# Performance work log

Hardware: AMD Instinct MI355X
Metric: run time of the kernel (lower is better)

The kernel has to match this reference:

```python
import jax, jax.numpy as jnp
import numpy as np

B = 128; DIM_IN = 3; MAX_CYCLE = 50; NODES = 18
T = MAX_CYCLE * NODES          # cycle_size = 900
F1, F2 = 32, 64                # stgcn_filters
NCLS = 3
N = B * T                      # nodes seen by GATv2 = 115200
E = 12 * N                     # edges (avg degree 12)
EPS = 1e-5


def setup_inputs() -> dict:
    key = jax.random.key(0)
    keys = iter(jax.random.split(key, 48))
    def p(shape, scale=0.05):
        return jax.random.normal(next(keys), shape, jnp.float32) * scale
    inp = {}
    inp["x"] = jax.random.normal(next(keys), (B, DIM_IN, T), jnp.float32)
    inp["edge_index"] = jax.random.randint(next(keys), (2, E), 0, N)
    def block(pfx, cin, c):
        inp[pfx + "_tc1_w"] = p((c, cin, 5)); inp[pfx + "_tc1_b"] = p((c,))
        inp[pfx + "_wl"] = p((c, c)); inp[pfx + "_bl"] = p((c,))
        inp[pfx + "_wr"] = p((c, c)); inp[pfx + "_br"] = p((c,))
        inp[pfx + "_att"] = p((c,)); inp[pfx + "_gbias"] = p((c,))
        inp[pfx + "_bn_g"] = jnp.ones((c,), jnp.float32)
        inp[pfx + "_bn_b"] = jnp.zeros((c,), jnp.float32)
        inp[pfx + "_tc2_w"] = p((c, c, 5)); inp[pfx + "_tc2_b"] = p((c,))
    block("b1", DIM_IN, F1)
    block("b2", F1, F2)
    inp["fc1_w"] = p((128, T * F2), 0.01); inp["fc1_b"] = p((128,))
    inp["hbn1_g"] = jnp.ones((128,), jnp.float32); inp["hbn1_b"] = jnp.zeros((128,), jnp.float32)
    inp["fc2_w"] = p((64, 128)); inp["fc2_b"] = p((64,))
    inp["hbn2_g"] = jnp.ones((64,), jnp.float32); inp["hbn2_b"] = jnp.zeros((64,), jnp.float32)
    inp["fc3_w"] = p((NCLS, 64)); inp["fc3_b"] = p((NCLS,))
    return inp


def _conv1d_same(x, w, b):
    # x: [B, Cin, T], w: [Cout, Cin, 5], 'same' padding (pad 2/2)
    y = jax.lax.conv_general_dilated(x, w, (1,), [(2, 2)],
                                     dimension_numbers=("NCH", "OIH", "NCH"))
    return y + b[None, :, None]


def _bn(h, g, b):
    # BatchNorm1d on [N, C] with batch statistics
    m = h.mean(0)
    v = h.var(0)
    return (h - m) * jax.lax.rsqrt(v + EPS) * g + b


def _gatv2(h, src, dst, wl, bl, wr, br, att, gbias):
    # PyG GATv2Conv, heads=1, negative_slope=0.2, self loops already in src/dst
    xl = h @ wl.T + bl            # source transform, also the message
    xr = h @ wr.T + br            # target transform
    e = jnp.dot(jax.nn.leaky_relu(xl[src] + xr[dst], 0.2), att)  # [E]
    m = jax.ops.segment_max(e, dst, num_segments=N)
    ex = jnp.exp(e - m[dst])
    s = jax.ops.segment_sum(ex, dst, num_segments=N)
    alpha = ex / s[dst]
    out = jax.ops.segment_sum(alpha[:, None] * xl[src], dst, num_segments=N)
    return out + gbias


def _block(x, src, dst, tc1_w, tc1_b, wl, bl, wr, br, att, gbias, bn_g, bn_b, tc2_w, tc2_b):
    x = jax.nn.relu(_conv1d_same(x, tc1_w, tc1_b))      # [B, C, T]
    C = tc1_w.shape[0]
    h = x.reshape(T * B, C)                             # torch .view(T*B, C) (raw row-major)
    h = jax.nn.relu(_gatv2(h, src, dst, wl, bl, wr, br, att, gbias))
    h = _bn(h, bn_g, bn_b)
    h = h.reshape(B, C, T)                              # torch .view(B, C, T)
    return jax.nn.relu(_conv1d_same(h, tc2_w, tc2_b))


def reference(x, edge_index,
              b1_tc1_w, b1_tc1_b, b1_wl, b1_bl, b1_wr, b1_br, b1_att, b1_gbias,
              b1_bn_g, b1_bn_b, b1_tc2_w, b1_tc2_b,
              b2_tc1_w, b2_tc1_b, b2_wl, b2_bl, b2_wr, b2_br, b2_att, b2_gbias,
              b2_bn_g, b2_bn_b, b2_tc2_w, b2_tc2_b,
              fc1_w, fc1_b, hbn1_g, hbn1_b, fc2_w, fc2_b, hbn2_g, hbn2_b, fc3_w, fc3_b):
    sl = jnp.arange(N, dtype=edge_index.dtype)          # PyG add_self_loops=True
    src = jnp.concatenate([edge_index[0], sl])
    dst = jnp.concatenate([edge_index[1], sl])
    h = _block(x, src, dst, b1_tc1_w, b1_tc1_b, b1_wl, b1_bl, b1_wr, b1_br,
               b1_att, b1_gbias, b1_bn_g, b1_bn_b, b1_tc2_w, b1_tc2_b)
    h = jax.nn.relu(h)                                  # extra relu on non-final block (dropout off)
    h = _block(h, src, dst, b2_tc1_w, b2_tc1_b, b2_wl, b2_bl, b2_wr, b2_br,
               b2_att, b2_gbias, b2_bn_g, b2_bn_b, b2_tc2_w, b2_tc2_b)
    h = h.reshape(B, F2 * T)
    h = jax.nn.relu(h @ fc1_w.T + fc1_b)
    h = _bn(h, hbn1_g, hbn1_b)
    h = jax.nn.relu(h @ fc2_w.T + fc2_b)
    h = _bn(h, hbn2_g, hbn2_b)
    logits = h @ fc3_w.T + fc3_b
    return (jax.nn.sigmoid(logits), logits)
```

## Files before the change

### kernel.cpp

```cpp
#include <hip/hip_runtime.h>
#include <hip/hip_bf16.h>

typedef __hip_bfloat16 bf16;
typedef __attribute__((ext_vector_type(8))) short s16x8;
typedef __attribute__((ext_vector_type(4))) float f32x4;
#define DEV static __device__ __forceinline__

DEV float b2f(bf16 v){ return __bfloat162float(v); }
DEV bf16  f2b(float v){ return __float2bfloat16(v); }
DEV int   is_f32(const void* gones){ return ((const unsigned int*)gones)[0] == 0x3F800000u ? 1 : 0; }
DEV float ldin(const void* p, int f32, int i){
    return f32 ? ((const float*)p)[i] : __bfloat162float(((const bf16*)p)[i]);
}
DEV void unpk(unsigned u, float& a, float& b){
    a = __uint_as_float(u << 16);
    b = __uint_as_float(u & 0xffff0000u);
}
DEV float lrelu(float t){ return fmaxf(t, 0.f) + 0.2f * fminf(t, 0.f); }
DEV unsigned short bfu(float v){ bf16 h = f2b(v); return *(unsigned short*)&h; }
DEV float ldT(const float* p, int i){ return p[i]; }
DEV float ldT(const bf16*  p, int i){ return b2f(p[i]); }
DEV void st4(float* d, float4 o){ *(float4*)d = o; }
DEV void st1(float* d, float v){ *d = v; }
DEV void st4(bf16* d, float4 o){
    unsigned short ob[4] = {bfu(o.x), bfu(o.y), bfu(o.z), bfu(o.w)};
    *(ushort4*)d = *(ushort4*)ob;
}
DEV void st1(bf16* d, float v){ *d = f2b(v); }

constexpr int Bb  = 128;
constexpr int Tt  = 900;
constexpr int Nn  = Bb * Tt;
constexpr int Ee  = 12 * Nn;
constexpr int CAP = 48;
constexpr int NBK  = 256;
constexpr int NPB  = Nn / NBK;
constexpr int BCAP = 8192;
constexpr int WROWS = 96 + 1024 + 2048 + 4096;
constexpr int WTOT  = WROWS * 5;
constexpr int WBF   = 5120 + 10240 + 20480;
constexpr int WXT   = 2*32*32 + 64 + 2*64*64 + 128;

__global__ __launch_bounds__(256) void k_wprep(const void* wa, const void* wb_, const void* wc,
    const void* wd,
    const void* b1wl, const void* b1bl, const void* b1wr, const void* b1br,
    const void* b2wl, const void* b2bl, const void* b2wr, const void* b2br,
    const void* gones, float* __restrict__ wp, bf16* __restrict__ wbf,
    float* __restrict__ wx, int* __restrict__ gcur){
    const int f32 = is_f32(gones);
    if (blockIdx.x == 0 && threadIdx.x < NBK) gcur[threadIdx.x] = 0;
    int e = blockIdx.x * 256 + threadIdx.x;
    if (e < WTOT){
        int r = e / 5, k = e - r * 5;
        const void* src; int rb;
        if (r < 96)      { src = wa; rb = 0; }
        else if (r < 1120){ src = wb_; rb = 96; }
        else if (r < 3168){ src = wc; rb = 1120; }
        else             { src = wd; rb = 3168; }
        wp[r * 8 + k] = ldin(src, f32, (r - rb) * 5 + k);
    } else if (e < WTOT + WBF){
        int e2 = e - WTOT;
        const void* src; int kk, r;
        if (e2 < 5120)      { kk = e2 >> 10; r = e2 & 1023; src = wb_; }
        else if (e2 < 15360){ int e3 = e2 - 5120;  kk = e3 >> 11; r = e3 & 2047; src = wc; }
        else                { int e3 = e2 - 15360; kk = e3 >> 12; r = e3 & 4095; src = wd; }
        wbf[e2] = f2b(ldin(src, f32, r * 5 + kk));
    } else if (e < WTOT + WBF + WXT){
        int e3 = e - WTOT - WBF;
        float v;
        if      (e3 < 1024){ int t = e3;         int c = t >> 5, f = t & 31; v = ldin(b1wl, f32, f * 32 + c); }
        else if (e3 < 2048){ int t = e3 - 1024;  int c = t >> 5, f = t & 31; v = ldin(b1wr, f32, f * 32 + c); }
        else if (e3 < 2080)  v = ldin(b1bl, f32, e3 - 2048);
        else if (e3 < 2112)  v = ldin(b1br, f32, e3 - 2080);
        else if (e3 < 6208){ int t = e3 - 2112;  int c = t >> 6, f = t & 63; v = ldin(b2wl, f32, f * 64 + c); }
        else if (e3 < 10304){int t = e3 - 6208;  int c = t >> 6, f = t & 63; v = ldin(b2wr, f32, f * 64 + c); }
        else if (e3 < 10368) v = ldin(b2bl, f32, e3 - 10304);
        else                 v = ldin(b2br, f32, e3 - 10368);
        wx[e3] = v;
    }
}

__global__ __launch_bounds__(256) void k_bucket(const int* __restrict__ ei,
                                                int* __restrict__ gcur, int2* __restrict__ bkt){
    constexpr int TILE = 4096;
    const int base = blockIdx.x * TILE;
    const int tid = threadIdx.x;
    __shared__ int cnt[NBK];
    __shared__ int gbase[NBK];
    cnt[tid] = 0;
    __syncthreads();
    int es[16], er[16], eb[16], rk[16];
    #pragma unroll
    for (int k = 0; k < 16; ++k){
        int idx = base + k * 256 + tid;
        if (idx < Ee){
            es[k] = ei[idx];
            int d = ei[Ee + idx];
            eb[k] = d / NPB;
            er[k] = d - eb[k] * NPB;
            rk[k] = atomicAdd(&cnt[eb[k]], 1);
        } else eb[k] = -1;
    }
    __syncthreads();
    {
        int c = cnt[tid];
        gbase[tid] = (c > 0) ? atomicAdd(&gcur[tid], c) : 0;
    }
    __syncthreads();
    #pragma unroll
    for (int k = 0; k < 16; ++k){
        if (eb[k] >= 0){
            int slot = gbase[eb[k]] + rk[k];
            if (slot < BCAP)
                bkt[(size_t)eb[k] * BCAP + slot] = make_int2(er[k], es[k]);
        }
    }
}

__global__ __launch_bounds__(256) void k_csr2(const int2* __restrict__ bkt, const int* __restrict__ gcur,
                                              int* __restrict__ csr, int* __restrict__ cnt){
    const int b = blockIdx.x;
    const int n0 = b * NPB;
    __shared__ int lcnt[NPB];
    for (int i = threadIdx.x; i < NPB; i += 256) lcnt[i] = 0;
    __syncthreads();
    const int tot = min(gcur[b], BCAP);
    for (int i = threadIdx.x; i < tot; i += 256){
        int2 e = bkt[(size_t)b * BCAP + i];
        int p = atomicAdd(&lcnt[e.x], 1);
        if (p < CAP) csr[(size_t)(n0 + e.x) * CAP + p] = e.y;
    }
    __syncthreads();
    for (int i = threadIdx.x; i < NPB; i += 256) cnt[n0 + i] = lcnt[i];
}

template<bool EXT, int CIN, int COUT, bool BN>
__global__ __launch_bounds__(256) void k_conv(const void* __restrict__ x,
    const float* __restrict__ wp, int wbase,
    const void* __restrict__ bias, const float* __restrict__ scale, const float* __restrict__ shift,
    const void* __restrict__ gones, float* __restrict__ y)
{
    const int f32 = is_f32(gones);
    __shared__ alignas(16) float xs[CIN][132];
    const int b = blockIdx.x >> 3, t0 = (blockIdx.x & 7) * 128;
    const int tid = threadIdx.x;
    for (int i = tid; i < CIN * 132; i += 256){
        int ci = i / 132, tt = i % 132;
        int gt = t0 + tt - 2;
        float v = 0.f;
        if (gt >= 0 && gt < Tt){
            int idx = (b * CIN + ci) * Tt + gt;
            v = EXT ? ldin(x, f32, idx) : ((const float*)x)[idx];
            if (BN){
                int f = (ci * (Tt % CIN) + gt) % CIN;
                v = v * scale[f] + shift[f];
            }
        }
        xs[ci][tt] = v;
    }
    __syncthreads();
    constexpr int HALF = COUT / 2;
    constexpr int NT   = 256 / HALF;
    constexpr int NW   = 128 / (NT * 4);
    const int cop = tid / NT;
    const int tch = tid % NT;
    const int co = cop, co2 = cop + HALF;
    float acc[NW][2][4];
    #pragma unroll
    for (int iw = 0; iw < NW; ++iw)
        #pragma unroll
        for (int h = 0; h < 2; ++h)
            #pragma unroll
            for (int j = 0; j < 4; ++j) acc[iw][h][j] = 0.f;

    const float* w0p = wp + (size_t)(wbase + co  * CIN) * 8;
    const float* w1p = wp + (size_t)(wbase + co2 * CIN) * 8;
    float4 na = *(const float4*)w0p; float na4 = w0p[4];
    float4 nb = *(const float4*)w1p; float nb4 = w1p[4];
    for (int ci = 0; ci < CIN; ++ci){
        const float w0[5] = {na.x, na.y, na.z, na.w, na4};
        const float w1[5] = {nb.x, nb.y, nb.z, nb.w, nb4};
        if (ci + 1 < CIN){
            const float* p0 = w0p + (size_t)(ci + 1) * 8;
            const float* p1 = w1p + (size_t)(ci + 1) * 8;
            na = *(const float4*)p0; na4 = p0[4];
            nb = *(const float4*)p1; nb4 = p1[4];
        }
        #pragma unroll
        for (int iw = 0; iw < NW; ++iw){
            const int tl = tch * 4 + iw * NT * 4;
            float4 a  = *(const float4*)&xs[ci][tl];
            float4 bq = *(const float4*)&xs[ci][tl + 4];
            float xw[8] = {a.x,a.y,a.z,a.w,bq.x,bq.y,bq.z,bq.w};
            #pragma unroll
            for (int k = 0; k < 5; ++k)
                #pragma unroll
                for (int j = 0; j < 4; ++j){
                    acc[iw][0][j] = fmaf(xw[j + k], w0[k], acc[iw][0][j]);
                    acc[iw][1][j] = fmaf(xw[j + k], w1[k], acc[iw][1][j]);
                }
        }
    }
    const float bv0 = ldin(bias, f32, co), bv1 = ldin(bias, f32, co2);
    #pragma unroll
    for (int iw = 0; iw < NW; ++iw){
        const int t = t0 + tch * 4 + iw * NT * 4;
        if (t < Tt){
            float4 o0, o1;
            o0.x = fmaxf(acc[iw][0][0] + bv0, 0.f); o0.y = fmaxf(acc[iw][0][1] + bv0, 0.f);
            o0.z = fmaxf(acc[iw][0][2] + bv0, 0.f); o0.w = fmaxf(acc[iw][0][3] + bv0, 0.f);
            o1.x = fmaxf(acc[iw][1][0] + bv1, 0.f); o1.y = fmaxf(acc[iw][1][1] + bv1, 0.f);
            o1.z = fmaxf(acc[iw][1][2] + bv1, 0.f); o1.w = fmaxf(acc[iw][1][3] + bv1, 0.f);
            *(float4*)&y[(b * COUT + co ) * Tt + t] = o0;
            *(float4*)&y[(b * COUT + co2) * Tt + t] = o1;
        }
    }
}

template<typename TI, typename TO, int CIN, int COUT, bool BN>
__global__ __launch_bounds__(256) void k_convM(const TI* __restrict__ x, const bf16* __restrict__ wbf,
    int wbase,
    const void* __restrict__ bias, const float* __restrict__ scale, const float* __restrict__ shift,
    const void* __restrict__ gones, TO* __restrict__ y)
{
    const int f32 = is_f32(gones);
    constexpr int STR = CIN + 8;
    constexpr int CI2 = CIN / 2;
    __shared__ alignas(16) float smem[COUT * 132];
    unsigned short* xsT = (unsigned short*)smem;
    const int b = blockIdx.x >> 3, t0 = (blockIdx.x & 7) * 128;
    const int tid = threadIdx.x;
    for (int i = tid; i < CI2 * 128; i += 256){
        int ci2 = i >> 7, tt = i & 127;
        int gt = t0 + tt - 2;
        int ci = ci2 * 2;
        unsigned pack = 0;
        if (gt >= 0 && gt < Tt){
            float v0 = ldT(x, (b * CIN + ci) * Tt + gt);
            float v1 = ldT(x, (b * CIN + ci + 1) * Tt + gt);
            if (BN){
                int fa = (4 * ci + gt) & (CIN - 1), fb = (4 * ci + 4 + gt) & (CIN - 1);
                v0 = v0 * scale[fa] + shift[fa];
                v1 = v1 * scale[fb] + shift[fb];
            }
            pack = (unsigned)bfu(v0) | ((unsigned)bfu(v1) << 16);
        }
        *(unsigned*)&xsT[tt * STR + ci] = pack;
    }
    if (tid < CI2 * 4){
        int ci2 = tid >> 2, tt = 128 + (tid & 3);
        int gt = t0 + tt - 2;
        int ci = ci2 * 2;
        unsigned pack = 0;
        if (gt < Tt){
            float v0 = ldT(x, (b * CIN + ci) * Tt + gt);
            float v1 = ldT(x, (b * CIN + ci + 1) * Tt + gt);
            if (BN){
                int fa = (4 * ci + gt) & (CIN - 1), fb = (4 * ci + 4 + gt) & (CIN - 1);
                v0 = v0 * scale[fa] + shift[fa];
                v1 = v1 * scale[fb] + shift[fb];
            }
            pack = (unsigned)bfu(v0) | ((unsigned)bfu(v1) << 16);
        }
        *(unsigned*)&xsT[tt * STR + ci] = pack;
    }
    __syncthreads();
    const int lane = tid & 63, wid = tid >> 6;
    const int l15 = lane & 15, quad = lane >> 4;
    constexpr int MT  = COUT / 16;
    constexpr int NTP = 2 * MT;
    const int mt  = (MT == 4) ? wid : (wid & 1);
    const int ntb = (MT == 4) ? 0 : (wid >> 1) * NTP;
    const int co0 = mt * 16;
    f32x4 acc[NTP];
    #pragma unroll
    for (int nt = 0; nt < NTP; ++nt){ f32x4 z = {0.f, 0.f, 0.f, 0.f}; acc[nt] = z; }
    for (int kk = 0; kk < 5; ++kk){
        #pragma unroll
        for (int kb = 0; kb < CIN / 32; ++kb){
            s16x8 a = *(const s16x8*)&wbf[wbase + kk * (COUT * CIN) + (co0 + l15) * CIN + kb * 32 + quad * 8];
            #pragma unroll
            for (int nt = 0; nt < NTP; ++nt){
                s16x8 bf = *(const s16x8*)&xsT[((ntb + nt) * 16 + l15 + kk) * STR + kb * 32 + quad * 8];
                acc[nt] = __builtin_amdgcn_mfma_f32_16x16x32_bf16(a, bf, acc[nt], 0, 0, 0);
            }
        }
    }
    __syncthreads();
    #pragma unroll
    for (int nt = 0; nt < NTP; ++nt)
        #pragma unroll
        for (int r = 0; r < 4; ++r)
            smem[(co0 + quad * 4 + r) * 132 + (ntb + nt) * 16 + l15] = acc[nt][r];
    __syncthreads();
    for (int i = tid; i < COUT * 32; i += 256){
        int co = i >> 5, c4 = (i & 31) << 2;
        int t = t0 + c4;
        if (t < Tt){
            float4 o = *(float4*)&smem[co * 132 + c4];
            float bb = ldin(bias, f32, co);
            o.x = fmaxf(o.x + bb, 0.f); o.y = fmaxf(o.y + bb, 0.f);
            o.z = fmaxf(o.z + bb, 0.f); o.w = fmaxf(o.w + bb, 0.f);
            TO* dst = &y[(size_t)(b * COUT + co) * Tt + t];
            if (t + 3 < Tt) st4(dst, o);
            else {
                float ov[4] = {o.x, o.y, o.z, o.w};
                for (int j = 0; j < 4 && t + j < Tt; ++j) st1(dst + j, ov[j]);
            }
        }
    }
}

template<int C>
__global__ __launch_bounds__(256) void k_xlxr(const float* __restrict__ h,
    const float* __restrict__ wx, int wxoff,
    unsigned short* __restrict__ xlh, float* __restrict__ xr,
    double* __restrict__ bnp)
{
    constexpr int NB = 4096 / C;
    constexpr int HS = NB + 4;
    __shared__ alignas(16) float hT[C][HS];
    __shared__ alignas(16) float wlS[C * C];
    __shared__ alignas(16) float wrS[C * C];
    const int tid = threadIdx.x;
    const int n0 = blockIdx.x * NB;
    if (blockIdx.x == 0){
        for (int i = tid; i < 256 * 2 * C; i += 256) bnp[i] = 0.0;
    }
    for (int i = tid; i < NB * C; i += 256){
        int n = i & (NB - 1), c = i / NB;
        hT[c][n] = h[(size_t)(n0 + n) * C + c];
    }
    const float* wl = wx + wxoff;
    const float* wr = wl + C * C;
    for (int i = tid; i < C * C; i += 256){
        wlS[i] = wl[i];
        wrS[i] = wr[i];
    }
    __syncthreads();
    const float* bl = wr + C * C;
    const float* br = bl + C;
    constexpr int FG = C / 4;
    const int fg = tid % FG, ng = tid / FG;
    const int nloc = ng * 4, floc = fg * 4;
    float blv[4], brv[4];
    #pragma unroll
    for (int j = 0; j < 4; ++j){ blv[j] = bl[floc + j]; brv[j] = br[floc + j]; }
    float accL[4][4], accR[4][4];
    #pragma unroll
    for (int i = 0; i < 4; ++i)
        #pragma unroll
        for (int j = 0; j < 4; ++j){ accL[i][j] = 0.f; accR[i][j] = 0.f; }
    #pragma unroll 4
    for (int c = 0; c < C; ++c){
        float4 hv = *(const float4*)&hT[c][nloc];
        float4 lv = *(const float4*)&wlS[c * C + floc];
        float4 rv = *(const float4*)&wrS[c * C + floc];
        float ha[4] = {hv.x,hv.y,hv.z,hv.w};
        float la[4] = {lv.x,lv.y,lv.z,lv.w};
        float ra[4] = {rv.x,rv.y,rv.z,rv.w};
        #pragma unroll
        for (int i = 0; i < 4; ++i)
            #pragma unroll
            for (int j = 0; j < 4; ++j){
                accL[i][j] = fmaf(ha[i], la[j], accL[i][j]);
                accR[i][j] = fmaf(ha[i], ra[j], accR[i][j]);
            }
    }
    #pragma unroll
    for (int i = 0; i < 4; ++i){
        size_t n = n0 + nloc + i;
        bf16 hb[4];
        hb[0] = f2b(accL[i][0] + blv[0]); hb[1] = f2b(accL[i][1] + blv[1]);
        hb[2] = f2b(accL[i][2] + blv[2]); hb[3] = f2b(accL[i][3] + blv[3]);
        *(ushort4*)&xlh[n * C + floc] = *(ushort4*)hb;
        float4 r;
        r.x = accR[i][0] + brv[0]; r.y = accR[i][1] + brv[1];
        r.z = accR[i][2] + brv[2]; r.w = accR[i][3] + brv[3];
        *(float4*)&xr[n * C + floc] = r;
    }
}

template<int L> DEV float rsumL(float v){
    #pragma unroll
    for (int s = L / 2; s > 0; s >>= 1) v += __shfl_xor(v, s, 64);
    return v;
}

template<int C, int FPL>
__global__ __launch_bounds__(256) void k_gat(const unsigned short* __restrict__ xlh,
    const float* __restrict__ xr,
    const int* __restrict__ csr, const int* __restrict__ cnt,
    const void* __restrict__ att, const void* __restrict__ gbias,
    const void* __restrict__ gones, float* __restrict__ out,
    double* __restrict__ bnp)
{
    const int f32 = is_f32(gones);
    constexpr int L   = C / FPL;
    constexpr int NPW = 64 / L;
    const int lane = threadIdx.x & 63, wid = threadIdx.x >> 6;
    const int sub = lane / L, fp = lane % L;
    const int node = (blockIdx.x * 4 + wid) * NPW + sub;
    const int f0 = FPL * fp;
    float xrv[FPL], a1v[FPL], a2v[FPL];
    if constexpr (FPL == 4){
        float4 t = *(const float4*)&xr[(size_t)node * C + f0];
        xrv[0] = t.x; xrv[1] = t.y; xrv[2] = t.z; xrv[3] = t.w;
    } else {
        float2 t = *(const float2*)&xr[(size_t)node * C + f0];
        xrv[0] = t.x; xrv[1] = t.y;
    }
    #pragma unroll
    for (int i = 0; i < FPL; ++i){
        float a = ldin(att, f32, f0 + i);
        a1v[i] = 0.6f * a;
        a2v[i] = 0.4f * a;
    }
    const int deg = min(cnt[node], CAP);
    int degu = deg;
    #pragma unroll
    for (int s = L; s < 64; s <<= 1) degu = max(degu, __shfl_xor(degu, s, 64));

    auto loadv = [&](int s, float (&v)[FPL]){
        if constexpr (FPL == 4){
            uint2 u = *(const uint2*)&xlh[(size_t)s * C + f0];
            unpk(u.x, v[0], v[1]); unpk(u.y, v[2], v[3]);
        } else {
            unsigned u = *(const unsigned*)&xlh[(size_t)s * C + f0];
            unpk(u, v[0], v[1]);
        }
    };
    auto score = [&](const float (&v)[FPL]){
        float l = 0.f;
        #pragma unroll
        for (int i = 0; i < FPL; ++i){
            float t = v[i] + xrv[i];
            l = fmaf(a1v[i], t, l);
            l = fmaf(a2v[i], fabsf(t), l);
        }
        return rsumL<L>(l);
    };

    float ssum, acc[FPL];
    {
        float v[FPL];
        loadv(node, v);
        float w = __expf(score(v));
        ssum = w;
        #pragma unroll
        for (int i = 0; i < FPL; ++i) acc[i] = w * v[i];
    }
    for (int j = 0; j < degu; j += 8){
        const int* crow = &csr[(size_t)node * CAP + j];
        int4 sa = *(const int4*)crow;
        int4 sb = *(const int4*)(crow + 4);
        int ss[8] = {sa.x, sa.y, sa.z, sa.w, sb.x, sb.y, sb.z, sb.w};
        bool av[8];
        #pragma unroll
        for (int q = 0; q < 8; ++q){
            av[q] = (j + q < deg);
            if (!av[q]) ss[q] = node;
        }
        float v[8][FPL];
        #pragma unroll
        for (int q = 0; q < 8; ++q) loadv(ss[q], v[q]);
        float e[8];
        #pragma unroll
        for (int q = 0; q < 8; ++q) e[q] = score(v[q]);
        #pragma unroll
        for (int q = 0; q < 8; ++q){
            float w = av[q] ? __expf(e[q]) : 0.f;
            ssum += w;
            #pragma unroll
            for (int i = 0; i < FPL; ++i) acc[i] = fmaf(w, v[q][i], acc[i]);
        }
    }
    float inv = 1.f / ssum;
    float ov[FPL];
    #pragma unroll
    for (int i = 0; i < FPL; ++i)
        ov[i] = fmaxf(fmaf(acc[i], inv, ldin(gbias, f32, f0 + i)), 0.f);
    if constexpr (FPL == 4){
        float4 o; o.x = ov[0]; o.y = ov[1]; o.z = ov[2]; o.w = ov[3];
        *(float4*)&out[(size_t)node * C + f0] = o;
    } else {
        float2 o; o.x = ov[0]; o.y = ov[1];
        *(float2*)&out[(size_t)node * C + f0] = o;
    }
    float s1[FPL], s2[FPL];
    #pragma unroll
    for (int i = 0; i < FPL; ++i){ s1[i] = ov[i]; s2[i] = ov[i] * ov[i]; }
    #pragma unroll
    for (int s = L; s < 64; s <<= 1){
        #pragma unroll
        for (int i = 0; i < FPL; ++i){
            s1[i] += __shfl_xor(s1[i], s, 64);
            s2[i] += __shfl_xor(s2[i], s, 64);
        }
    }
    __shared__ float wred[4][2][C];
    if (sub == 0){
        #pragma unroll
        for (int i = 0; i < FPL; ++i){
            wred[wid][0][f0 + i] = s1[i];
            wred[wid][1][f0 + i] = s2[i];
        }
    }
    __syncthreads();
    const int tid = threadIdx.x;
    if (tid < 2 * C){
        const int stat = tid >= C, f = tid - stat * C;
        float t = (wred[0][stat][f] + wred[1][stat][f]) + (wred[2][stat][f] + wred[3][stat][f]);
        atomicAdd(&bnp[(size_t)(blockIdx.x & 255) * 2 * C + stat * C + f], (double)t);
    }
}

template<int C>
__global__ void k_bnstat2(const double* __restrict__ part, const void* __restrict__ g,
                          const void* __restrict__ b, const void* __restrict__ gones,
                          float* __restrict__ scale, float* __restrict__ shift){
    const int f32 = is_f32(gones);
    const int f = threadIdx.x;
    double s1 = 0.0, s2 = 0.0;
    for (int s = 0; s < 256; ++s){ s1 += part[s * 2 * C + f]; s2 += part[s * 2 * C + C + f]; }
    double mean = s1 / (double)Nn;
    double var  = s2 / (double)Nn - mean * mean;
    float sc = (float)((double)ldin(g, f32, f) / sqrt(var + 1e-5));
    float sh = ldin(b, f32, f) - (float)mean * sc;
    scale[f] = sc; shift[f] = sh;
}

__global__ __launch_bounds__(256) void k_fc1(const float* __restrict__ h, const void* __restrict__ w1,
                                             const void* __restrict__ gones, float* __restrict__ part){
    const int f32 = is_f32(gones);
    __shared__ alignas(16) float AT[32][136];
    __shared__ alignas(16) float BT[32][136];
    const int tid = threadIdx.x;
    const int blk = blockIdx.x;
    const int k0 = blk * 128;
    const int bg = tid >> 4, jg = tid & 15;
    const int row = tid >> 5, kk = tid & 31;
    float ar[16], br[16];
    #pragma unroll
    for (int q = 0; q < 16; ++q){
        int idx = (row + q * 8) * 57600 + k0 + kk;
        ar[q] = h[idx];
        br[q] = ldin(w1, f32, idx);
    }
    float acc[8][8];
    #pragma unroll
    for (int i = 0; i < 8; ++i)
        #pragma unroll
        for (int j = 0; j < 8; ++j) acc[i][j] = 0.f;
    for (int ch = 0; ch < 4; ++ch){
        __syncthreads();
        #pragma unroll
        for (int q = 0; q < 16; ++q){
            AT[kk][row + q * 8] = ar[q];
            BT[kk][row + q * 8] = br[q];
        }
        __syncthreads();
        if (ch < 3){
            const int kb = k0 + (ch + 1) * 32;
            #pragma unroll
            for (int q = 0; q < 16; ++q){
                int idx = (row + q * 8) * 57600 + kb + kk;
                ar[q] = h[idx];
                br[q] = ldin(w1, f32, idx);
            }
        }
        for (int k2 = 0; k2 < 32; ++k2){
            float4 a0 = *(const float4*)&AT[k2][bg * 8];
            float4 a1 = *(const float4*)&AT[k2][bg * 8 + 4];
            float4 c0 = *(const float4*)&BT[k2][jg * 8];
            float4 c1 = *(const float4*)&BT[k2][jg * 8 + 4];
            float av[8] = {a0.x,a0.y,a0.z,a0.w,a1.x,a1.y,a1.z,a1.w};
            float bv[8] = {c0.x,c0.y,c0.z,c0.w,c1.x,c1.y,c1.z,c1.w};
            #pragma unroll
            for (int i = 0; i < 8; ++i)
                #pragma unroll
                for (int j = 0; j < 8; ++j) acc[i][j] = fmaf(av[i], bv[j], acc[i][j]);
        }
    }
    #pragma unroll
    for (int i = 0; i < 8; ++i){
        int bb = bg * 8 + i;
        #pragma unroll
        for (int q = 0; q < 2; ++q){
            float4 o;
            o.x = acc[i][q*4+0]; o.y = acc[i][q*4+1]; o.z = acc[i][q*4+2]; o.w = acc[i][q*4+3];
            *(float4*)&part[blk * 16384 + bb * 128 + jg * 8 + q * 4] = o;
        }
    }
}

__global__ void k_fc1red1(const float* __restrict__ part, float* __restrict__ pr2){
    const int y = blockIdx.x >> 6;
    const int o = (blockIdx.x & 63) * 256 + threadIdx.x;
    const int sb0 = y * 57;
    const int sb1 = min(sb0 + 57, 450);
    float s = 0.f;
    for (int sb = sb0; sb < sb1; ++sb) s += part[(size_t)sb * 16384 + o];
    pr2[(size_t)y * 16384 + o] = s;
}

__global__ void k_fc1red2(const float* __restrict__ pr2, const void* __restrict__ bias,
                          const void* __restrict__ gones, float* __restrict__ out1){
    const int f32 = is_f32(gones);
    const int o = blockIdx.x * 256 + threadIdx.x;
    float s = ldin(bias, f32, o & 127);
    #pragma unroll
    for (int y = 0; y < 8; ++y) s += pr2[(size_t)y * 16384 + o];
    out1[o] = fmaxf(s, 0.f);
}

__global__ void k_hstat(const float* __restrict__ out1, const void* __restrict__ g1,
                        const void* __restrict__ b1, const void* __restrict__ gones,
                        float* __restrict__ sc, float* __restrict__ sh){
    const int f32 = is_f32(gones);
    const int f = threadIdx.x;
    double s1 = 0.0, s2 = 0.0;
    for (int r = 0; r < 128; ++r){ float v = out1[r * 128 + f]; s1 += v; s2 += (double)v * v; }
    double mean = s1 / 128.0, var = s2 / 128.0 - mean * mean;
    float s = (float)((double)ldin(g1, f32, f) / sqrt(var + 1e-5));
    sc[f] = s;
    sh[f] = ldin(b1, f32, f) - (float)mean * s;
}

__global__ __launch_bounds__(256) void k_fc2(const float* __restrict__ out1,
    const float* __restrict__ sc, const float* __restrict__ sh,
    const void* __restrict__ w2, const void* __restrict__ fb2,
    const void* __restrict__ gones, float* __restrict__ f2)
{
    const int f32 = is_f32(gones);
    __shared__ alignas(16) float hs[4 * 128];
    __shared__ alignas(16) float w2s[64 * 132];
    const int tid = threadIdx.x;
    const int b0 = blockIdx.x * 4;
    for (int i = tid; i < 512; i += 256){
        int f = i & 127;
        hs[i] = out1[b0 * 128 + i] * sc[f] + sh[f];
    }
    for (int i = tid; i < 8192; i += 256)
        w2s[(i >> 7) * 132 + (i & 127)] = ldin(w2, f32, i);
    __syncthreads();
    const int b = tid >> 6, o = tid & 63;
    float acc = ldin(fb2, f32, o);
    const float* hp = &hs[b * 128];
    const float* wq = &w2s[o * 132];
    #pragma unroll
    for (int k = 0; k < 128; k += 4){
        float4 hv = *(const float4*)&hp[k];
        float4 wv = *(const float4*)&wq[k];
        acc = fmaf(hv.x, wv.x, acc); acc = fmaf(hv.y, wv.y, acc);
        acc = fmaf(hv.z, wv.z, acc); acc = fmaf(hv.w, wv.w, acc);
    }
    f2[(b0 + b) * 64 + o] = fmaxf(acc, 0.f);
}

__global__ __launch_bounds__(256) void k_head2(const float* __restrict__ f2,
    const void* g2, const void* b2v, const void* w3, const void* fb3,
    const void* gones, void* __restrict__ out)
{
    const int f32 = is_f32(gones);
    __shared__ float fs[8192];
    __shared__ float sc2[64], sh2[64];
    const int tid = threadIdx.x;
    for (int i = tid; i < 8192; i += 256) fs[i] = f2[i];
    __syncthreads();
    if (tid < 64){
        double s1 = 0.0, s2 = 0.0;
        for (int r = 0; r < 128; ++r){ float v = fs[r * 64 + tid]; s1 += v; s2 += (double)v * v; }
        double mean = s1 / 128.0, var = s2 / 128.0 - mean * mean;
        sc2[tid] = (float)((double)ldin(g2, f32, tid) / sqrt(var + 1e-5));
        sh2[tid] = ldin(b2v, f32, tid) - (float)mean * sc2[tid];
    }
    __syncthreads();
    if (tid < 128){
        float hv[64];
        for (int k = 0; k < 64; ++k) hv[k] = fs[tid * 64 + k] * sc2[k] + sh2[k];
        #pragma unroll
        for (int c = 0; c < 3; ++c){
            float acc = ldin(fb3, f32, c);
            for (int k = 0; k < 64; ++k) acc = fmaf(hv[k], ldin(w3, f32, c * 64 + k), acc);
            float sg = 1.f / (1.f + __expf(-acc));
            if (f32){
                ((float*)out)[384 + tid * 3 + c] = acc;
                ((float*)out)[tid * 3 + c] = sg;
            } else {
                ((bf16*)out)[384 + tid * 3 + c] = f2b(acc);
                ((bf16*)out)[tid * 3 + c] = f2b(sg);
            }
        }
    }
}

extern "C" void kernel_launch(void* const* d_in, const int* in_sizes, int n_in,
                              void* d_out, int out_size, void* d_ws, size_t ws_size,
                              hipStream_t stream)
{
    const void* x   = d_in[0];
    const int*  ei  = (const int*)d_in[1];
    const void* b1_tc1_w=d_in[2];  const void* b1_tc1_b=d_in[3];
    const void* b1_wl   =d_in[4];  const void* b1_bl   =d_in[5];
    const void* b1_wr   =d_in[6];  const void* b1_br   =d_in[7];
    const void* b1_att  =d_in[8];  const void* b1_gb   =d_in[9];
    const void* b1_g    =d_in[10]; const void* b1_bt   =d_in[11];
    const void* b1_tc2_w=d_in[12]; const void* b1_tc2_b=d_in[13];
    const void* b2_tc1_w=d_in[14]; const void* b2_tc1_b=d_in[15];
    const void* b2_wl   =d_in[16]; const void* b2_bl   =d_in[17];
    const void* b2_wr   =d_in[18]; const void* b2_br   =d_in[19];
    const void* b2_att  =d_in[20]; const void* b2_gb   =d_in[21];
    const void* b2_g    =d_in[22]; const void* b2_bt   =d_in[23];
    const void* b2_tc2_w=d_in[24]; const void* b2_tc2_b=d_in[25];
    const void* fc1_w=d_in[26]; const void* fc1_b=d_in[27];
    const void* hbn1_g=d_in[28]; const void* hbn1_b=d_in[29];
    const void* fc2_w=d_in[30]; const void* fc2_b=d_in[31];
    const void* hbn2_g=d_in[32]; const void* hbn2_b=d_in[33];
    const void* fc3_w=d_in[34]; const void* fc3_b=d_in[35];
    const void* gones = b1_g;

    float* ws = (float*)d_ws;
    const size_t NC = (size_t)Nn * 64;
    float* buf0 = ws;
    float* buf1 = ws + NC;
    float* buf2 = ws + 2 * NC;
    int*   csr  = (int*)(ws + 3 * NC);
    int*   cnt  = (int*)((char*)csr + (size_t)Nn * CAP * 4);
    double* bnp = (double*)((char*)cnt + (size_t)Nn * 4);
    float* scale = (float*)(bnp + 32768);
    float* shift = scale + 128;
    unsigned short* xlh = (unsigned short*)(shift + 128);
    int*   gcur = (int*)(xlh + (size_t)Nn * 64);
    float* wp   = (float*)(gcur + NBK);
    bf16*  wbf  = (bf16*)(wp + (size_t)WROWS * 8);
    float* wx   = (float*)(wbf + WBF);
    int2*  bkt  = (int2*)buf2;
    bf16*  c32o = (bf16*)buf0;
    float* part = buf0;
    float* out1 = buf2;
    float* pr2  = buf2 + 16384;
    float* f2b_ = pr2 + 8 * 16384;
    float* hsc  = f2b_ + 8192;
    float* hsh  = hsc + 128;

    k_wprep <<<(WTOT + WBF + WXT + 255) / 256, 256, 0, stream>>>(
        b1_tc1_w, b1_tc2_w, b2_tc1_w, b2_tc2_w,
        b1_wl, b1_bl, b1_wr, b1_br, b2_wl, b2_bl, b2_wr, b2_br,
        gones, wp, wbf, wx, gcur);
    k_bucket<<<(Ee + 4095) / 4096, 256, 0, stream>>>(ei, gcur, bkt);
    k_csr2  <<<NBK, 256, 0, stream>>>(bkt, gcur, csr, cnt);

    k_conv<true, 3, 32, false><<<Bb * 8, 256, 0, stream>>>(x, wp, 0, b1_tc1_b, nullptr, nullptr, gones, buf0);
    k_xlxr<32><<<Nn / 128, 256, 0, stream>>>(buf0, wx, 0, xlh, buf1, bnp);
    k_gat<32, 4><<<Nn / 32, 256, 0, stream>>>(xlh, buf1, csr, cnt, b1_att, b1_gb, gones, buf2, bnp);
    k_bnstat2<32><<<1, 32, 0, stream>>>(bnp, b1_g, b1_bt, gones, scale, shift);
    k_convM<float, bf16, 32, 32, true><<<Bb * 8, 256, 0, stream>>>(buf2, wbf, 0, b1_tc2_b, scale, shift, gones, c32o);

    k_convM<bf16, float, 32, 64, false><<<Bb * 8, 256, 0, stream>>>(c32o, wbf, 5120, b2_tc1_b, nullptr, nullptr, gones, buf1);
    k_xlxr<64><<<Nn / 64, 256, 0, stream>>>(buf1, wx, 2112, xlh, buf2, bnp);
    k_gat<64, 4><<<Nn / 16, 256, 0, stream>>>(xlh, buf2, csr, cnt, b2_att, b2_gb, gones, buf0, bnp);
    k_bnstat2<64><<<1, 64, 0, stream>>>(bnp, b2_g, b2_bt, gones, scale, shift);
    k_convM<float, float, 64, 64, true><<<Bb * 8, 256, 0, stream>>>(buf0, wbf, 15360, b2_tc2_b, scale, shift, gones, buf1);

    k_fc1<<<450, 256, 0, stream>>>(buf1, fc1_w, gones, part);
    k_fc1red1<<<512, 256, 0, stream>>>(part, pr2);
    k_fc1red2<<<64, 256, 0, stream>>>(pr2, fc1_b, gones, out1);
    k_hstat<<<1, 128, 0, stream>>>(out1, hbn1_g, hbn1_b, gones, hsc, hsh);
    k_fc2<<<32, 256, 0, stream>>>(out1, hsc, hsh, fc2_w, fc2_b, gones, f2b_);
    k_head2<<<1, 256, 0, stream>>>(f2b_, hbn2_g, hbn2_b, fc3_w, fc3_b, gones, d_out);
}
```

Measured before the change: 478.6 us.

## Merge independent graph-build kernels with conv/xlxr and halve fc1 split-K blocks

Edge bucketing now runs in the same launch as the first temporal conv, with blocks dispatched by index, and CSR build shares a launch with the block-1 xl/xr projection. Independent work overlaps and there are fewer kernel launches. Separately, fc1 now gives each block 256 K-columns instead of 128, halving the partial sums written and reduced. The merged kernels use more shared memory per block, and fewer fc1 blocks may leave some compute units idle.

```diff
diff --git a/kernel.cpp b/kernel.cpp
--- a/kernel.cpp
+++ b/kernel.cpp
@@ -36,10 +36,12 @@
 constexpr int NBK  = 256;
 constexpr int NPB  = Nn / NBK;
 constexpr int BCAP = 8192;
+constexpr int NBUB = (Ee + 4095) / 4096;
 constexpr int WROWS = 96 + 1024 + 2048 + 4096;
 constexpr int WTOT  = WROWS * 5;
 constexpr int WBF   = 5120 + 10240 + 20480;
 constexpr int WXT   = 2*32*32 + 64 + 2*64*64 + 128;
+constexpr int FCB   = 225;
 
 __global__ __launch_bounds__(256) void k_wprep(const void* wa, const void* wb_, const void* wc,
     const void* wd,
@@ -80,139 +82,191 @@
     }
 }
 
-__global__ __launch_bounds__(256) void k_bucket(const int* __restrict__ ei,
-                                                int* __restrict__ gcur, int2* __restrict__ bkt){
-    constexpr int TILE = 4096;
-    const int base = blockIdx.x * TILE;
+__global__ __launch_bounds__(256) void k_convbkt(const void* __restrict__ x,
+    const float* __restrict__ wp, const void* __restrict__ bias,
+    const void* __restrict__ gones, float* __restrict__ y,
+    const int* __restrict__ ei, int* __restrict__ gcur, int2* __restrict__ bkt)
+{
     const int tid = threadIdx.x;
-    __shared__ int cnt[NBK];
-    __shared__ int gbase[NBK];
-    cnt[tid] = 0;
-    __syncthreads();
-    int es[16], er[16], eb[16], rk[16];
-    #pragma unroll
-    for (int k = 0; k < 16; ++k){
-        int idx = base + k * 256 + tid;
-        if (idx < Ee){
-            es[k] = ei[idx];
-            int d = ei[Ee + idx];
-            eb[k] = d / NPB;
-            er[k] = d - eb[k] * NPB;
-            rk[k] = atomicAdd(&cnt[eb[k]], 1);
-        } else eb[k] = -1;
-    }
-    __syncthreads();
-    {
-        int c = cnt[tid];
-        gbase[tid] = (c > 0) ? atomicAdd(&gcur[tid], c) : 0;
-    }
-    __syncthreads();
-    #pragma unroll
-    for (int k = 0; k < 16; ++k){
-        if (eb[k] >= 0){
-            int slot = gbase[eb[k]] + rk[k];
-            if (slot < BCAP)
-                bkt[(size_t)eb[k] * BCAP + slot] = make_int2(er[k], es[k]);
-        }
-    }
-}
-
-__global__ __launch_bounds__(256) void k_csr2(const int2* __restrict__ bkt, const int* __restrict__ gcur,
-                                              int* __restrict__ csr, int* __restrict__ cnt){
-    const int b = blockIdx.x;
-    const int n0 = b * NPB;
-    __shared__ int lcnt[NPB];
-    for (int i = threadIdx.x; i < NPB; i += 256) lcnt[i] = 0;
-    __syncthreads();
-    const int tot = min(gcur[b], BCAP);
-    for (int i = threadIdx.x; i < tot; i += 256){
-        int2 e = bkt[(size_t)b * BCAP + i];
-        int p = atomicAdd(&lcnt[e.x], 1);
-        if (p < CAP) csr[(size_t)(n0 + e.x) * CAP + p] = e.y;
-    }
-    __syncthreads();
-    for (int i = threadIdx.x; i < NPB; i += 256) cnt[n0 + i] = lcnt[i];
-}
-
-template<bool EXT, int CIN, int COUT, bool BN>
-__global__ __launch_bounds__(256) void k_conv(const void* __restrict__ x,
-    const float* __restrict__ wp, int wbase,
-    const void* __restrict__ bias, const float* __restrict__ scale, const float* __restrict__ shift,
-    const void* __restrict__ gones, float* __restrict__ y)
+    if (blockIdx.x < Bb * 8){
+        const int f32 = is_f32(gones);
+        __shared__ alignas(16) float xs[3][132];
+        const int b = blockIdx.x >> 3, t0 = (blockIdx.x & 7) * 128;
+        for (int i = tid; i < 3 * 132; i += 256){
+            int ci = i / 132, tt = i % 132;
+            int gt = t0 + tt - 2;
+            float v = 0.f;
+            if (gt >= 0 && gt < Tt) v = ldin(x, f32, (b * 3 + ci) * Tt + gt);
+            xs[ci][tt] = v;
+        }
+        __syncthreads();
+        const int cop = tid / 16, tch = tid % 16;
+        const int co = cop, co2 = cop + 16;
+        float acc[2][2][4];
+        #pragma unroll
+        for (int iw = 0; iw < 2; ++iw)
+            #pragma unroll
+            for (int h = 0; h < 2; ++h)
+                #pragma unroll
+                for (int j = 0; j < 4; ++j) acc[iw][h][j] = 0.f;
+        const float* w0p = wp + (size_t)(co  * 3) * 8;
+        const float* w1p = wp + (size_t)(co2 * 3) * 8;
+        float4 na = *(const float4*)w0p; float na4 = w0p[4];
+        float4 nb = *(const float4*)w1p; float nb4 = w1p[4];
+        for (int ci = 0; ci < 3; ++ci){
+            const float w0[5] = {na.x, na.y, na.z, na.w, na4};
+            const float w1[5] = {nb.x, nb.y, nb.z, nb.w, nb4};
+            if (ci + 1 < 3){
+                const float* p0 = w0p + (size_t)(ci + 1) * 8;
+                const float* p1 = w1p + (size_t)(ci + 1) * 8;
+                na = *(const float4*)p0; na4 = p0[4];
+                nb = *(const float4*)p1; nb4 = p1[4];
+            }
+            #pragma unroll
+            for (int iw = 0; iw < 2; ++iw){
+                const int tl = tch * 4 + iw * 64;
+                float4 a  = *(const float4*)&xs[ci][tl];
+                float4 bq = *(const float4*)&xs[ci][tl + 4];
+                float xw[8] = {a.x,a.y,a.z,a.w,bq.x,bq.y,bq.z,bq.w};
+                #pragma unroll
+                for (int k = 0; k < 5; ++k)
+                    #pragma unroll
+                    for (int j = 0; j < 4; ++j){
+                        acc[iw][0][j] = fmaf(xw[j + k], w0[k], acc[iw][0][j]);
+                        acc[iw][1][j] = fmaf(xw[j + k], w1[k], acc[iw][1][j]);
+                    }
+            }
+        }
+        const float bv0 = ldin(bias, f32, co), bv1 = ldin(bias, f32, co2);
+        #pragma unroll
+        for (int iw = 0; iw < 2; ++iw){
+            const int t = t0 + tch * 4 + iw * 64;
+            if (t < Tt){
+                float4 o0, o1;
+                o0.x = fmaxf(acc[iw][0][0] + bv0, 0.f); o0.y = fmaxf(acc[iw][0][1] + bv0, 0.f);
+                o0.z = fmaxf(acc[iw][0][2] + bv0, 0.f); o0.w = fmaxf(acc[iw][0][3] + bv0, 0.f);
+                o1.x = fmaxf(acc[iw][1][0] + bv1, 0.f); o1.y = fmaxf(acc[iw][1][1] + bv1, 0.f);
+                o1.z = fmaxf(acc[iw][1][2] + bv1, 0.f); o1.w = fmaxf(acc[iw][1][3] + bv1, 0.f);
+                *(float4*)&y[(b * 32 + co ) * Tt + t] = o0;
+                *(float4*)&y[(b * 32 + co2) * Tt + t] = o1;
+            }
+        }
+    } else {
+        const int base = (int)(blockIdx.x - Bb * 8) * 4096;
+        __shared__ int cnt[NBK];
+        __shared__ int gbase[NBK];
+        cnt[tid] = 0;
+        __syncthreads();
+        int es[16], er[16], eb[16], rk[16];
+        #pragma unroll
+        for (int k = 0; k < 16; ++k){
+            int idx = base + k * 256 + tid;
+            if (idx < Ee){
+                es[k] = ei[idx];
+                int d = ei[Ee + idx];
+                eb[k] = d / NPB;
+                er[k] = d - eb[k] * NPB;
+                rk[k] = atomicAdd(&cnt[eb[k]], 1);
+            } else eb[k] = -1;
+        }
+        __syncthreads();
+        {
+            int c = cnt[tid];
+            gbase[tid] = (c > 0) ? atomicAdd(&gcur[tid], c) : 0;
+        }
+        __syncthreads();
+        #pragma unroll
+        for (int k = 0; k < 16; ++k){
+            if (eb[k] >= 0){
+                int slot = gbase[eb[k]] + rk[k];
+                if (slot < BCAP)
+                    bkt[(size_t)eb[k] * BCAP + slot] = make_int2(er[k], es[k]);
+            }
+        }
+    }
+}
+
+__global__ __launch_bounds__(256) void k_csr2xlxr(const int2* __restrict__ bkt,
+    const int* __restrict__ gcur, int* __restrict__ csr, int* __restrict__ cnt,
+    const float* __restrict__ h, const float* __restrict__ wx, int wxoff,
+    unsigned short* __restrict__ xlh, float* __restrict__ xr, double* __restrict__ bnp)
 {
-    const int f32 = is_f32(gones);
-    __shared__ alignas(16) float xs[CIN][132];
-    const int b = blockIdx.x >> 3, t0 = (blockIdx.x & 7) * 128;
     const int tid = threadIdx.x;
-    for (int i = tid; i < CIN * 132; i += 256){
-        int ci = i / 132, tt = i % 132;
-        int gt = t0 + tt - 2;
-        float v = 0.f;
-        if (gt >= 0 && gt < Tt){
-            int idx = (b * CIN + ci) * Tt + gt;
-            v = EXT ? ldin(x, f32, idx) : ((const float*)x)[idx];
-            if (BN){
-                int f = (ci * (Tt % CIN) + gt) % CIN;
-                v = v * scale[f] + shift[f];
-            }
-        }
-        xs[ci][tt] = v;
-    }
-    __syncthreads();
-    constexpr int HALF = COUT / 2;
-    constexpr int NT   = 256 / HALF;
-    constexpr int NW   = 128 / (NT * 4);
-    const int cop = tid / NT;
-    const int tch = tid % NT;
-    const int co = cop, co2 = cop + HALF;
-    float acc[NW][2][4];
-    #pragma unroll
-    for (int iw = 0; iw < NW; ++iw)
-        #pragma unroll
-        for (int h = 0; h < 2; ++h)
+    if (blockIdx.x < NBK){
+        const int b = blockIdx.x;
+        const int n0 = b * NPB;
+        __shared__ int lcnt[NPB];
+        for (int i = tid; i < NPB; i += 256) lcnt[i] = 0;
+        __syncthreads();
+        const int tot = min(gcur[b], BCAP);
+        for (int i = tid; i < tot; i += 256){
+            int2 e = bkt[(size_t)b * BCAP + i];
+            int p = atomicAdd(&lcnt[e.x], 1);
+            if (p < CAP) csr[(size_t)(n0 + e.x) * CAP + p] = e.y;
+        }
+        __syncthreads();
+        for (int i = tid; i < NPB; i += 256) cnt[n0 + i] = lcnt[i];
+    } else {
+        constexpr int C = 32, NB = 128, HS = 132;
+        __shared__ alignas(16) float hT[C][HS];
+        __shared__ alignas(16) float wlS[C * C];
+        __shared__ alignas(16) float wrS[C * C];
+        const int bx = (int)blockIdx.x - NBK;
+        const int n0 = bx * NB;
+        if (bx == 0){
+            for (int i = tid; i < 256 * 2 * C; i += 256) bnp[i] = 0.0;
+        }
+        for (int i = tid; i < NB * C; i += 256){
+            int n = i & (NB - 1), c = i / NB;
+            hT[c][n] = h[(size_t)(n0 + n) * C + c];
+        }
+        const float* wl = wx + wxoff;
+        const float* wr = wl + C * C;
+        for (int i = tid; i < C * C; i += 256){
+            wlS[i] = wl[i];
+            wrS[i] = wr[i];
+        }
+        __syncthreads();
+        const float* bl = wr + C * C;
+        const float* br = bl + C;
+        constexpr int FG = C / 4;
+        const int fg = tid % FG, ng = tid / FG;
+        const int nloc = ng * 4, floc = fg * 4;
+        float blv[4], brv[4];
+        #pragma unroll
+        for (int j = 0; j < 4; ++j){ blv[j] = bl[floc + j]; brv[j] = br[floc + j]; }
+        float accL[4][4], accR[4][4];
+        #pragma unroll
+        for (int i = 0; i < 4; ++i)
             #pragma unroll
-            for (int j = 0; j < 4; ++j) acc[iw][h][j] = 0.f;
-
-    const float* w0p = wp + (size_t)(wbase + co  * CIN) * 8;
-    const float* w1p = wp + (size_t)(wbase + co2 * CIN) * 8;
-    float4 na = *(const float4*)w0p; float na4 = w0p[4];
-    float4 nb = *(const float4*)w1p; float nb4 = w1p[4];
-    for (int ci = 0; ci < CIN; ++ci){
-        const float w0[5] = {na.x, na.y, na.z, na.w, na4};
-        const float w1[5] = {nb.x, nb.y, nb.z, nb.w, nb4};
-        if (ci + 1 < CIN){
-            const float* p0 = w0p + (size_t)(ci + 1) * 8;
-            const float* p1 = w1p + (size_t)(ci + 1) * 8;
-            na = *(const float4*)p0; na4 = p0[4];
-            nb = *(const float4*)p1; nb4 = p1[4];
-        }
-        #pragma unroll
-        for (int iw = 0; iw < NW; ++iw){
-            const int tl = tch * 4 + iw * NT * 4;
-            float4 a  = *(const float4*)&xs[ci][tl];
-            float4 bq = *(const float4*)&xs[ci][tl + 4];
-            float xw[8] = {a.x,a.y,a.z,a.w,bq.x,bq.y,bq.z,bq.w};
+            for (int j = 0; j < 4; ++j){ accL[i][j] = 0.f; accR[i][j] = 0.f; }
+        #pragma unroll 4
+        for (int c = 0; c < C; ++c){
+            float4 hv = *(const float4*)&hT[c][nloc];
+            float4 lv = *(const float4*)&wlS[c * C + floc];
+            float4 rv = *(const float4*)&wrS[c * C + floc];
+            float ha[4] = {hv.x,hv.y,hv.z,hv.w};
+            float la[4] = {lv.x,lv.y,lv.z,lv.w};
+            float ra[4] = {rv.x,rv.y,rv.z,rv.w};
             #pragma unroll
-            for (int k = 0; k < 5; ++k)
+            for (int i = 0; i < 4; ++i)
                 #pragma unroll
                 for (int j = 0; j < 4; ++j){
-                    acc[iw][0][j] = fmaf(xw[j + k], w0[k], acc[iw][0][j]);
-                    acc[iw][1][j] = fmaf(xw[j + k], w1[k], acc[iw][1][j]);
+                    accL[i][j] = fmaf(ha[i], la[j], accL[i][j]);
+                    accR[i][j] = fmaf(ha[i], ra[j], accR[i][j]);
                 }
         }
-    }
-    const float bv0 = ldin(bias, f32, co), bv1 = ldin(bias, f32, co2);
-    #pragma unroll
-    for (int iw = 0; iw < NW; ++iw){
-        const int t = t0 + tch * 4 + iw * NT * 4;
-        if (t < Tt){
-            float4 o0, o1;
-            o0.x = fmaxf(acc[iw][0][0] + bv0, 0.f); o0.y = fmaxf(acc[iw][0][1] + bv0, 0.f);
-            o0.z = fmaxf(acc[iw][0][2] + bv0, 0.f); o0.w = fmaxf(acc[iw][0][3] + bv0, 0.f);
-            o1.x = fmaxf(acc[iw][1][0] + bv1, 0.f); o1.y = fmaxf(acc[iw][1][1] + bv1, 0.f);
-            o1.z = fmaxf(acc[iw][1][2] + bv1, 0.f); o1.w = fmaxf(acc[iw][1][3] + bv1, 0.f);
-            *(float4*)&y[(b * COUT + co ) * Tt + t] = o0;
-            *(float4*)&y[(b * COUT + co2) * Tt + t] = o1;
+        #pragma unroll
+        for (int i = 0; i < 4; ++i){
+            size_t n = n0 + nloc + i;
+            bf16 hb[4];
+            hb[0] = f2b(accL[i][0] + blv[0]); hb[1] = f2b(accL[i][1] + blv[1]);
+            hb[2] = f2b(accL[i][2] + blv[2]); hb[3] = f2b(accL[i][3] + blv[3]);
+            *(ushort4*)&xlh[n * C + floc] = *(ushort4*)hb;
+            float4 r;
+            r.x = accR[i][0] + brv[0]; r.y = accR[i][1] + brv[1];
+            r.z = accR[i][2] + brv[2]; r.w = accR[i][3] + brv[3];
+            *(float4*)&xr[n * C + floc] = r;
         }
     }
 }
@@ -537,7 +591,7 @@
     __shared__ alignas(16) float BT[32][136];
     const int tid = threadIdx.x;
     const int blk = blockIdx.x;
-    const int k0 = blk * 128;
+    const int k0 = blk * 256;
     const int bg = tid >> 4, jg = tid & 15;
     const int row = tid >> 5, kk = tid & 31;
     float ar[16], br[16];
@@ -552,7 +606,7 @@
     for (int i = 0; i < 8; ++i)
         #pragma unroll
         for (int j = 0; j < 8; ++j) acc[i][j] = 0.f;
-    for (int ch = 0; ch < 4; ++ch){
+    for (int ch = 0; ch < 8; ++ch){
         __syncthreads();
         #pragma unroll
         for (int q = 0; q < 16; ++q){
@@ -560,7 +614,7 @@
             BT[kk][row + q * 8] = br[q];
         }
         __syncthreads();
-        if (ch < 3){
+        if (ch < 7){
             const int kb = k0 + (ch + 1) * 32;
             #pragma unroll
             for (int q = 0; q < 16; ++q){
@@ -597,8 +651,8 @@
 __global__ void k_fc1red1(const float* __restrict__ part, float* __restrict__ pr2){
     const int y = blockIdx.x >> 6;
     const int o = (blockIdx.x & 63) * 256 + threadIdx.x;
-    const int sb0 = y * 57;
-    const int sb1 = min(sb0 + 57, 450);
+    const int sb0 = y * 29;
+    const int sb1 = min(sb0 + 29, FCB);
     float s = 0.f;
     for (int sb = sb0; sb < sb1; ++sb) s += part[(size_t)sb * 16384 + o];
     pr2[(size_t)y * 16384 + o] = s;
@@ -748,11 +802,9 @@
         b1_tc1_w, b1_tc2_w, b2_tc1_w, b2_tc2_w,
         b1_wl, b1_bl, b1_wr, b1_br, b2_wl, b2_bl, b2_wr, b2_br,
         gones, wp, wbf, wx, gcur);
-    k_bucket<<<(Ee + 4095) / 4096, 256, 0, stream>>>(ei, gcur, bkt);
-    k_csr2  <<<NBK, 256, 0, stream>>>(bkt, gcur, csr, cnt);
-
-    k_conv<true, 3, 32, false><<<Bb * 8, 256, 0, stream>>>(x, wp, 0, b1_tc1_b, nullptr, nullptr, gones, buf0);
-    k_xlxr<32><<<Nn / 128, 256, 0, stream>>>(buf0, wx, 0, xlh, buf1, bnp);
+
+    k_convbkt<<<Bb * 8 + NBUB, 256, 0, stream>>>(x, wp, b1_tc1_b, gones, buf0, ei, gcur, bkt);
+    k_csr2xlxr<<<NBK + Nn / 128, 256, 0, stream>>>(bkt, gcur, csr, cnt, buf0, wx, 0, xlh, buf1, bnp);
     k_gat<32, 4><<<Nn / 32, 256, 0, stream>>>(xlh, buf1, csr, cnt, b1_att, b1_gb, gones, buf2, bnp);
     k_bnstat2<32><<<1, 32, 0, stream>>>(bnp, b1_g, b1_bt, gones, scale, shift);
     k_convM<float, bf16, 32, 32, true><<<Bb * 8, 256, 0, stream>>>(buf2, wbf, 0, b1_tc2_b, scale, shift, gones, c32o);
@@ -763,7 +815,7 @@
     k_bnstat2<64><<<1, 64, 0, stream>>>(bnp, b2_g, b2_bt, gones, scale, shift);
     k_convM<float, float, 64, 64, true><<<Bb * 8, 256, 0, stream>>>(buf0, wbf, 15360, b2_tc2_b, scale, shift, gones, buf1);
 
-    k_fc1<<<450, 256, 0, stream>>>(buf1, fc1_w, gones, part);
+    k_fc1<<<FCB, 256, 0, stream>>>(buf1, fc1_w, gones, part);
     k_fc1red1<<<512, 256, 0, stream>>>(part, pr2);
     k_fc1red2<<<64, 256, 0, stream>>>(pr2, fc1_b, gones, out1);
     k_hstat<<<1, 128, 0, stream>>>(out1, hbn1_g, hbn1_b, gones, hsc, hsh);
```

Result: no change. 476.3 us (-0.5%).
